# Kernel tuning notes

Hardware: AMD Instinct MI355X
Metric: run time of the kernel (lower is better)

## Reference

```python
import jax, jax.numpy as jnp
import numpy as np


def gcn_conv(x, src, dst, deg_inv_sqrt, W, b):
    # PyG GCNConv: h = x @ W, then symmetric-normalized scatter-add over edges
    # (edge list already includes self-loops; deg computed over it).
    h = x @ W                                   # [N, F_out]
    norm = deg_inv_sqrt[src] * deg_inv_sqrt[dst]  # [E]
    msgs = h[src] * norm[:, None]               # gather + scale
    out = jax.ops.segment_sum(msgs, dst, num_segments=x.shape[0])
    return out + b


def setup_inputs() -> dict:
    key = jax.random.key(0)
    k1, k2, k3, k4 = jax.random.split(key, 4)
    N, E, F_in, F_hid, F_out = 200000, 6400000, 128, 8, 16
    x = jax.random.normal(k1, (N, F_in), dtype=jnp.float32)
    edge_index = jax.random.randint(k2, (2, E), 0, N, dtype=jnp.int64)
    W1 = jax.random.normal(k3, (F_in, F_hid), dtype=jnp.float32) * (1.0 / np.sqrt(F_in))
    b1 = jnp.zeros((F_hid,), dtype=jnp.float32)
    W2 = jax.random.normal(k4, (F_hid, F_out), dtype=jnp.float32) * (1.0 / np.sqrt(F_hid))
    b2 = jnp.zeros((F_out,), dtype=jnp.float32)
    return {"x": x, "edge_index": edge_index, "W1": W1, "b1": b1, "W2": W2, "b2": b2}


def reference(x, edge_index, W1, b1, W2, b2):
    N = x.shape[0]
    # add self-loops (GCNConv default add_self_loops=True)
    loops = jnp.arange(N, dtype=edge_index.dtype)
    src = jnp.concatenate([edge_index[0], loops])
    dst = jnp.concatenate([edge_index[1], loops])
    deg = jax.ops.segment_sum(jnp.ones_like(dst, dtype=x.dtype), dst, num_segments=N)
    deg_inv_sqrt = jnp.where(deg > 0, jax.lax.rsqrt(deg), 0.0)
    h = jax.nn.relu(gcn_conv(x, src, dst, deg_inv_sqrt, W1, b1))
    # dropout is identity in eval mode (training=False)
    out = gcn_conv(h, src, dst, deg_inv_sqrt, W2, b2)
    return out
```

## Files before the change

kernel.cpp:

```cpp
#include <hip/hip_runtime.h>
#include <hip/hip_fp16.h>

#define F_IN  128
#define F_HID 8
#define F_OUT 16

#define SBSH  9
#define SBW   (1 << SBSH)
#define MAXB  400
#define BIN_CAP  32
#define FLUSH_G  16


__global__ void init_gcur(int* __restrict__ gcur, int cap, int B) {
    int b = blockIdx.x * blockDim.x + threadIdx.x;
    if (b < B) gcur[b] = b * cap;
}

__global__ __launch_bounds__(512) void stage_bin(const int* __restrict__ ei,
                                                 int* __restrict__ gcur,
                                                 int* __restrict__ stage,
                                                 int E, int B, int per_block) {
    __shared__ int bin_cnt[MAXB];
    __shared__ int bin_buf[MAXB * BIN_CAP];
    for (int i = threadIdx.x; i < B; i += blockDim.x) bin_cnt[i] = 0;
    __syncthreads();
    const bool vec = ((E & 3) == 0);
    int base = blockIdx.x * per_block;
    int end  = min(E, base + per_block);
    for (int it = base; it < end; it += (int)blockDim.x * 4) {
        int e = it + (int)threadIdx.x * 4;
        int sv[4], dv[4], m4 = 0;
        if (vec && e + 3 < end) {
            int4 s4 = *(const int4*)(ei + e);
            int4 d4 = *(const int4*)(ei + E + e);
            sv[0] = s4.x; sv[1] = s4.y; sv[2] = s4.z; sv[3] = s4.w;
            dv[0] = d4.x; dv[1] = d4.y; dv[2] = d4.z; dv[3] = d4.w;
            m4 = 4;
        } else {
            for (int q = 0; e + q < end && q < 4; q++) { sv[q] = ei[e + q]; dv[q] = ei[E + e + q]; m4++; }
        }
        for (int q = 0; q < m4; q++) {
            int b   = dv[q] >> SBSH;
            int val = (sv[q] << SBSH) | (dv[q] & (SBW - 1));
            int pos = atomicAdd(&bin_cnt[b], 1);
            if (pos < BIN_CAP) {
                bin_buf[b * BIN_CAP + ((pos + b) & (BIN_CAP - 1))] = val;
            } else {
                int gp = atomicAdd(&gcur[b], 1);
                stage[gp] = val;
            }
        }
        __syncthreads();
        for (int b2 = threadIdx.x; b2 < B; b2 += blockDim.x) {
            int c = min(bin_cnt[b2], BIN_CAP);
            if (c >= FLUSH_G) {
                int m = c & ~(FLUSH_G - 1);
                int r = atomicAdd(&gcur[b2], m);
                for (int k = 0; k < m; k++)
                    stage[r + k] = bin_buf[b2 * BIN_CAP + ((k + b2) & (BIN_CAP - 1))];
                for (int k = m; k < c; k++)
                    bin_buf[b2 * BIN_CAP + ((k - m + b2) & (BIN_CAP - 1))] =
                        bin_buf[b2 * BIN_CAP + ((k + b2) & (BIN_CAP - 1))];
                bin_cnt[b2] = c - m;
            } else {
                bin_cnt[b2] = c;
            }
        }
        __syncthreads();
    }
    for (int b2 = threadIdx.x; b2 < B; b2 += blockDim.x) {
        int c = min(bin_cnt[b2], BIN_CAP);
        if (c > 0) {
            int r = atomicAdd(&gcur[b2], c);
            for (int k = 0; k < c; k++)
                stage[r + k] = bin_buf[b2 * BIN_CAP + ((k + b2) & (BIN_CAP - 1))];
        }
    }
}

__global__ __launch_bounds__(512) void scatter_csr(const int* __restrict__ stage,
                                                   const int* __restrict__ gcur,
                                                   int cap,
                                                   int* __restrict__ cnt,
                                                   float* __restrict__ dis,
                                                   int* __restrict__ row_start,
                                                   int* __restrict__ csr, int n) {
    __shared__ int s0[SBW], s1[SBW];
    int b  = blockIdx.x;
    int nb = b << SBSH;
    int i  = threadIdx.x;
    s0[i] = 0;
    __syncthreads();
    int base = b * cap;
    int num  = gcur[b] - base;
    for (int k = i; k < num; k += 512)
        atomicAdd(&s0[stage[base + k] & (SBW - 1)], 1);
    __syncthreads();
    int c = s0[i];
    if (nb + i < n) { cnt[nb + i] = c; dis[nb + i] = rsqrtf((float)(c + 1)); }
    int* src = s0; int* dst = s1;
    for (int off = 1; off < SBW; off <<= 1) {
        int v = src[i] + ((i >= off) ? src[i - off] : 0);
        dst[i] = v;
        __syncthreads();
        int* t = src; src = dst; dst = t;
    }
    int e = base + src[i] - c;
    if (nb + i < n) row_start[nb + i] = e;
    dst[i] = e;
    __syncthreads();
    for (int k = i; k < num; k += 512) {
        int v = stage[base + k];
        int pos = atomicAdd(&dst[v & (SBW - 1)], 1);
        csr[pos] = v >> SBSH;
    }
}

__global__ __launch_bounds__(256) void gemm1(const float* __restrict__ x,
                                             const float* __restrict__ W1,
                                             const float* __restrict__ dis,
                                             __half* __restrict__ g1, int n) {
    __shared__ float w[F_IN * F_HID];
    for (int i = threadIdx.x; i < F_IN * F_HID; i += blockDim.x) w[i] = W1[i];
    __syncthreads();
    int node = blockIdx.x * blockDim.x + threadIdx.x;
    if (node >= n) return;
    const float4* xr = (const float4*)(x + (size_t)node * F_IN);
    float acc[F_HID];
#pragma unroll
    for (int f = 0; f < F_HID; f++) acc[f] = 0.0f;
#pragma unroll
    for (int j = 0; j < F_IN / 4; j++) {
        float4 v = xr[j];
        const float* wr = &w[j * 4 * F_HID];
#pragma unroll
        for (int f = 0; f < F_HID; f++)
            acc[f] += v.x * wr[f] + v.y * wr[F_HID + f] + v.z * wr[2 * F_HID + f] + v.w * wr[3 * F_HID + f];
    }
    float d = dis[node];
    __half2 h[4];
#pragma unroll
    for (int p = 0; p < 4; p++) h[p] = __floats2half2_rn(acc[2 * p] * d, acc[2 * p + 1] * d);
    *(uint4*)(g1 + (size_t)node * F_HID) = *(uint4*)h;
}

__global__ __launch_bounds__(256) void aggregate_relu(const int* __restrict__ csr,
                                                      const int* __restrict__ row_start,
                                                      const int* __restrict__ cnt,
                                                      const float* __restrict__ dis,
                                                      const float* __restrict__ b1,
                                                      const __half* __restrict__ gin,
                                                      __half* __restrict__ gout, int n) {
    __shared__ float bb[F_HID];
    if (threadIdx.x < F_HID) bb[threadIdx.x] = b1[threadIdx.x];
    __syncthreads();
    int t = blockIdx.x * blockDim.x + threadIdx.x;
    int node = t >> 3;
    int f = t & 7;
    if (node >= n) return;
    int beg = row_start[node];
    int c   = cnt[node];
    float acc = __half2float(gin[(size_t)node * F_HID + f]);
    int j = 0;
    for (; j + 3 < c; j += 4) {
        int s0 = __builtin_nontemporal_load(csr + beg + j);
        int s1 = __builtin_nontemporal_load(csr + beg + j + 1);
        int s2 = __builtin_nontemporal_load(csr + beg + j + 2);
        int s3 = __builtin_nontemporal_load(csr + beg + j + 3);
        float a0 = __half2float(gin[(size_t)s0 * F_HID + f]);
        float a1 = __half2float(gin[(size_t)s1 * F_HID + f]);
        float a2 = __half2float(gin[(size_t)s2 * F_HID + f]);
        float a3 = __half2float(gin[(size_t)s3 * F_HID + f]);
        acc += (a0 + a1) + (a2 + a3);
    }
    for (; j < c; j++) {
        int s = __builtin_nontemporal_load(csr + beg + j);
        acc += __half2float(gin[(size_t)s * F_HID + f]);
    }
    float d = dis[node];
    float r = fmaxf(acc * d + bb[f], 0.0f) * d;
    gout[(size_t)node * F_HID + f] = __float2half(r);
}

__global__ __launch_bounds__(256) void aggregate_out(const int* __restrict__ csr,
                                                     const int* __restrict__ row_start,
                                                     const int* __restrict__ cnt,
                                                     const float* __restrict__ dis,
                                                     const float* __restrict__ W2,
                                                     const float* __restrict__ b2,
                                                     const __half* __restrict__ gin,
                                                     float* __restrict__ out, int n) {
    __shared__ float w[F_HID * F_OUT];
    __shared__ float bb[F_OUT];
    if (threadIdx.x < F_HID * F_OUT) w[threadIdx.x] = W2[threadIdx.x];
    if (threadIdx.x < F_OUT) bb[threadIdx.x] = b2[threadIdx.x];
    __syncthreads();
    int t = blockIdx.x * blockDim.x + threadIdx.x;
    int node = t >> 3;
    int f = t & 7;
    if (node >= n) return;
    int beg = row_start[node];
    int c   = cnt[node];
    float acc = __half2float(gin[(size_t)node * F_HID + f]);
    int j = 0;
    for (; j + 3 < c; j += 4) {
        int s0 = __builtin_nontemporal_load(csr + beg + j);
        int s1 = __builtin_nontemporal_load(csr + beg + j + 1);
        int s2 = __builtin_nontemporal_load(csr + beg + j + 2);
        int s3 = __builtin_nontemporal_load(csr + beg + j + 3);
        float a0 = __half2float(gin[(size_t)s0 * F_HID + f]);
        float a1 = __half2float(gin[(size_t)s1 * F_HID + f]);
        float a2 = __half2float(gin[(size_t)s2 * F_HID + f]);
        float a3 = __half2float(gin[(size_t)s3 * F_HID + f]);
        acc += (a0 + a1) + (a2 + a3);
    }
    for (; j < c; j++) {
        int s = __builtin_nontemporal_load(csr + beg + j);
        acc += __half2float(gin[(size_t)s * F_HID + f]);
    }
    float a_self = acc * dis[node];
    float o0 = bb[2 * f], o1 = bb[2 * f + 1];
#pragma unroll
    for (int k = 0; k < 8; k++) {
        float ak = __shfl(a_self, k, 8);
        o0 += ak * w[k * F_OUT + 2 * f];
        o1 += ak * w[k * F_OUT + 2 * f + 1];
    }
    *(float2*)(out + (size_t)node * F_OUT + 2 * f) = make_float2(o0, o1);
}

extern "C" void kernel_launch(void* const* d_in, const int* in_sizes, int n_in,
                              void* d_out, int out_size, void* d_ws, size_t ws_size,
                              hipStream_t stream) {
    const float* x  = (const float*)d_in[0];
    const int*   ei = (const int*)d_in[1];
    const float* W1 = (const float*)d_in[2];
    const float* b1 = (const float*)d_in[3];
    const float* W2 = (const float*)d_in[4];
    const float* b2 = (const float*)d_in[5];
    float* out = (float*)d_out;

    const int N = in_sizes[0] / F_IN;
    const int E = in_sizes[1] / 2;
    const int B = (N + SBW - 1) >> SBSH;

    int avg = (E + B - 1) / B;
    int cap = (avg + avg / 16 + 255) & ~255;

    int*    stage     = (int*)d_ws;
    int*    csr       = stage + (size_t)B * cap;
    float*  dis       = (float*)(csr + (size_t)B * cap);
    __half* gA        = (__half*)(dis + N);
    __half* gB        = (__half*)((int*)gA + (size_t)N * 4);
    int*    cnt       = (int*)gB + (size_t)N * 4;
    int*    row_start = cnt + N;
    int*    gcur      = row_start + N;

    const int BT = 256;
    dim3 blkN((N + BT - 1) / BT), thr(BT);
    dim3 blkA(((size_t)N * F_HID + BT - 1) / BT);

    int per_block = ((E + 639) / 640 + 2047) & ~2047;
    int SBLK = (E + per_block - 1) / per_block;

    init_gcur     <<<dim3((B + BT - 1) / BT), thr, 0, stream>>>(gcur, cap, B);
    stage_bin     <<<dim3(SBLK), dim3(512), 0, stream>>>(ei, gcur, stage, E, B, per_block);
    scatter_csr   <<<dim3(B),   dim3(512), 0, stream>>>(stage, gcur, cap, cnt, dis, row_start, csr, N);
    gemm1         <<<blkN, thr, 0, stream>>>(x, W1, dis, gA, N);
    aggregate_relu<<<blkA, thr, 0, stream>>>(csr, row_start, cnt, dis, b1, gA, gB, N);
    aggregate_out <<<blkA, thr, 0, stream>>>(csr, row_start, cnt, dis, W2, b2, gB, out, N);
}
```

Measured before the change: 462.7 us.

## Aggregate directly from binned edge buckets with LDS atomics instead of building CSR

Removes the CSR construction pass (prefix scan plus scatter into csr). Aggregation now streams each destination bucket's packed edges into LDS with double-buffered global_load_lds and accumulates into per-node LDS accumulators using workgroup-scope float atomics. The first GEMM now uses eight threads per node with shuffle reductions, and the degree pass reads int4 vectors. The trade is contended LDS atomics and one block per 512-node bucket, giving limited parallelism (about 391 blocks), in exchange for dropping a full edge-array write and read.

```diff
diff --git a/kernel.cpp b/kernel.cpp
--- a/kernel.cpp
+++ b/kernel.cpp
@@ -10,7 +10,10 @@
 #define MAXB  400
 #define BIN_CAP  32
 #define FLUSH_G  16
-
+#define TILE_E   2048
+
+
+typedef float f32x4 __attribute__((ext_vector_type(4)));
 
 __global__ void init_gcur(int* __restrict__ gcur, int cap, int B) {
     int b = blockIdx.x * blockDim.x + threadIdx.x;
@@ -79,155 +82,194 @@
     }
 }
 
-__global__ __launch_bounds__(512) void scatter_csr(const int* __restrict__ stage,
-                                                   const int* __restrict__ gcur,
-                                                   int cap,
-                                                   int* __restrict__ cnt,
-                                                   float* __restrict__ dis,
-                                                   int* __restrict__ row_start,
-                                                   int* __restrict__ csr, int n) {
-    __shared__ int s0[SBW], s1[SBW];
-    int b  = blockIdx.x;
-    int nb = b << SBSH;
-    int i  = threadIdx.x;
+__global__ __launch_bounds__(512) void degree_dis(const int* __restrict__ stage,
+                                                  const int* __restrict__ gcur,
+                                                  int cap, float* __restrict__ dis, int n) {
+    __shared__ int s0[SBW];
+    int b = blockIdx.x, i = threadIdx.x;
     s0[i] = 0;
     __syncthreads();
     int base = b * cap;
-    int num  = gcur[b] - base;
-    for (int k = i; k < num; k += 512)
+    int num  = min(gcur[b] - base, cap);
+    int numv = num & ~(TILE_E - 1);
+    for (int k = i * 4; k < numv; k += TILE_E) {
+        int4 v = *(const int4*)(stage + base + k);
+        atomicAdd(&s0[v.x & (SBW - 1)], 1);
+        atomicAdd(&s0[v.y & (SBW - 1)], 1);
+        atomicAdd(&s0[v.z & (SBW - 1)], 1);
+        atomicAdd(&s0[v.w & (SBW - 1)], 1);
+    }
+    for (int k = numv + i; k < num; k += 512)
         atomicAdd(&s0[stage[base + k] & (SBW - 1)], 1);
     __syncthreads();
-    int c = s0[i];
-    if (nb + i < n) { cnt[nb + i] = c; dis[nb + i] = rsqrtf((float)(c + 1)); }
-    int* src = s0; int* dst = s1;
-    for (int off = 1; off < SBW; off <<= 1) {
-        int v = src[i] + ((i >= off) ? src[i - off] : 0);
-        dst[i] = v;
-        __syncthreads();
-        int* t = src; src = dst; dst = t;
-    }
-    int e = base + src[i] - c;
-    if (nb + i < n) row_start[nb + i] = e;
-    dst[i] = e;
-    __syncthreads();
-    for (int k = i; k < num; k += 512) {
-        int v = stage[base + k];
-        int pos = atomicAdd(&dst[v & (SBW - 1)], 1);
-        csr[pos] = v >> SBSH;
-    }
+    int node = (b << SBSH) + i;
+    if (node < n) dis[node] = rsqrtf((float)(s0[i] + 1));
 }
 
 __global__ __launch_bounds__(256) void gemm1(const float* __restrict__ x,
                                              const float* __restrict__ W1,
                                              const float* __restrict__ dis,
                                              __half* __restrict__ g1, int n) {
-    __shared__ float w[F_IN * F_HID];
-    for (int i = threadIdx.x; i < F_IN * F_HID; i += blockDim.x) w[i] = W1[i];
-    __syncthreads();
-    int node = blockIdx.x * blockDim.x + threadIdx.x;
+    __shared__ float w2[F_HID * F_IN];
+    for (int i = threadIdx.x; i < F_HID * F_IN; i += blockDim.x) {
+        int f = i >> 7, k = i & (F_IN - 1);
+        w2[i] = W1[k * F_HID + f];
+    }
+    __syncthreads();
+    int t = blockIdx.x * blockDim.x + threadIdx.x;
+    int node = t >> 3, l = t & 7;
     if (node >= n) return;
-    const float4* xr = (const float4*)(x + (size_t)node * F_IN);
+    const f32x4* xr = (const f32x4*)(x + (size_t)node * F_IN);
     float acc[F_HID];
 #pragma unroll
     for (int f = 0; f < F_HID; f++) acc[f] = 0.0f;
 #pragma unroll
-    for (int j = 0; j < F_IN / 4; j++) {
-        float4 v = xr[j];
-        const float* wr = &w[j * 4 * F_HID];
-#pragma unroll
-        for (int f = 0; f < F_HID; f++)
-            acc[f] += v.x * wr[f] + v.y * wr[F_HID + f] + v.z * wr[2 * F_HID + f] + v.w * wr[3 * F_HID + f];
-    }
-    float d = dis[node];
-    __half2 h[4];
-#pragma unroll
-    for (int p = 0; p < 4; p++) h[p] = __floats2half2_rn(acc[2 * p] * d, acc[2 * p + 1] * d);
-    *(uint4*)(g1 + (size_t)node * F_HID) = *(uint4*)h;
-}
-
-__global__ __launch_bounds__(256) void aggregate_relu(const int* __restrict__ csr,
-                                                      const int* __restrict__ row_start,
-                                                      const int* __restrict__ cnt,
-                                                      const float* __restrict__ dis,
-                                                      const float* __restrict__ b1,
-                                                      const __half* __restrict__ gin,
-                                                      __half* __restrict__ gout, int n) {
+    for (int it = 0; it < 4; it++) {
+        int j = l + it * 8;
+        f32x4 v = xr[j];
+#pragma unroll
+        for (int f = 0; f < F_HID; f++) {
+            const float* wf = &w2[f * F_IN + j * 4];
+            acc[f] += v[0] * wf[0] + v[1] * wf[1] + v[2] * wf[2] + v[3] * wf[3];
+        }
+    }
+#pragma unroll
+    for (int f = 0; f < F_HID; f++) {
+        acc[f] += __shfl_xor(acc[f], 1);
+        acc[f] += __shfl_xor(acc[f], 2);
+        acc[f] += __shfl_xor(acc[f], 4);
+    }
+    if (l == 0) {
+        float d = dis[node];
+        __half2 h[4];
+#pragma unroll
+        for (int p = 0; p < 4; p++) h[p] = __floats2half2_rn(acc[2 * p] * d, acc[2 * p + 1] * d);
+        *(uint4*)(g1 + (size_t)node * F_HID) = *(uint4*)h;
+    }
+}
+
+__device__ __forceinline__ void gll16(const int* gsrc, int* ldst) {
+    __builtin_amdgcn_global_load_lds(
+        (const __attribute__((address_space(1))) void*)gsrc,
+        (__attribute__((address_space(3))) void*)ldst, 16, 0, 0);
+}
+
+__device__ __forceinline__ void lds_faddx(float* p, float v) {
+    (void)__hip_atomic_fetch_add(p, v, __ATOMIC_RELAXED, __HIP_MEMORY_SCOPE_WORKGROUP);
+}
+
+__device__ __forceinline__ void stage_tile(const int* __restrict__ stage, int base,
+                                           int t, int* lbuf, int tid) {
+    gll16(stage + base + t * TILE_E + tid * 4, lbuf + ((tid >> 6) << 8));
+}
+
+__device__ __forceinline__ void bucket_accumulate(const int* __restrict__ stage,
+                                                  int base, int num,
+                                                  const __half* __restrict__ gin,
+                                                  float* acc, int* ebuf, int tid) {
+    int ntile = (num + TILE_E - 1) / TILE_E;
+    if (ntile > 0) stage_tile(stage, base, 0, ebuf, tid);
+    int g = tid >> 3, f = tid & 7;
+    for (int t = 0; t < ntile; t++) {
+        int cur = t & 1;
+        __syncthreads();
+        if (t + 1 < ntile) stage_tile(stage, base, t + 1, ebuf + ((cur ^ 1) * TILE_E), tid);
+        int cnt_t = min(TILE_E, num - t * TILE_E);
+        const int* eb = ebuf + cur * TILE_E;
+        int k = g;
+        for (; k + 192 < cnt_t; k += 256) {
+            int v0 = eb[k], v1 = eb[k + 64], v2 = eb[k + 128], v3 = eb[k + 192];
+            float a0 = __half2float(gin[(size_t)((unsigned)v0 >> SBSH) * F_HID + f]);
+            float a1 = __half2float(gin[(size_t)((unsigned)v1 >> SBSH) * F_HID + f]);
+            float a2 = __half2float(gin[(size_t)((unsigned)v2 >> SBSH) * F_HID + f]);
+            float a3 = __half2float(gin[(size_t)((unsigned)v3 >> SBSH) * F_HID + f]);
+            lds_faddx(&acc[(v0 & (SBW - 1)) * F_HID + f], a0);
+            lds_faddx(&acc[(v1 & (SBW - 1)) * F_HID + f], a1);
+            lds_faddx(&acc[(v2 & (SBW - 1)) * F_HID + f], a2);
+            lds_faddx(&acc[(v3 & (SBW - 1)) * F_HID + f], a3);
+        }
+        for (; k < cnt_t; k += 64) {
+            int v = eb[k];
+            float a = __half2float(gin[(size_t)((unsigned)v >> SBSH) * F_HID + f]);
+            lds_faddx(&acc[(v & (SBW - 1)) * F_HID + f], a);
+        }
+    }
+    __syncthreads();
+}
+
+__global__ __launch_bounds__(512) void agg1(const int* __restrict__ stage,
+                                            const int* __restrict__ gcur, int cap,
+                                            const float* __restrict__ dis,
+                                            const float* __restrict__ b1,
+                                            const __half* __restrict__ gin,
+                                            __half* __restrict__ gout, int n) {
+    __shared__ __align__(16) float acc[SBW * F_HID];
+    __shared__ __align__(16) int   ebuf[2 * TILE_E];
     __shared__ float bb[F_HID];
-    if (threadIdx.x < F_HID) bb[threadIdx.x] = b1[threadIdx.x];
-    __syncthreads();
-    int t = blockIdx.x * blockDim.x + threadIdx.x;
-    int node = t >> 3;
-    int f = t & 7;
-    if (node >= n) return;
-    int beg = row_start[node];
-    int c   = cnt[node];
-    float acc = __half2float(gin[(size_t)node * F_HID + f]);
-    int j = 0;
-    for (; j + 3 < c; j += 4) {
-        int s0 = __builtin_nontemporal_load(csr + beg + j);
-        int s1 = __builtin_nontemporal_load(csr + beg + j + 1);
-        int s2 = __builtin_nontemporal_load(csr + beg + j + 2);
-        int s3 = __builtin_nontemporal_load(csr + beg + j + 3);
-        float a0 = __half2float(gin[(size_t)s0 * F_HID + f]);
-        float a1 = __half2float(gin[(size_t)s1 * F_HID + f]);
-        float a2 = __half2float(gin[(size_t)s2 * F_HID + f]);
-        float a3 = __half2float(gin[(size_t)s3 * F_HID + f]);
-        acc += (a0 + a1) + (a2 + a3);
-    }
-    for (; j < c; j++) {
-        int s = __builtin_nontemporal_load(csr + beg + j);
-        acc += __half2float(gin[(size_t)s * F_HID + f]);
-    }
-    float d = dis[node];
-    float r = fmaxf(acc * d + bb[f], 0.0f) * d;
-    gout[(size_t)node * F_HID + f] = __float2half(r);
-}
-
-__global__ __launch_bounds__(256) void aggregate_out(const int* __restrict__ csr,
-                                                     const int* __restrict__ row_start,
-                                                     const int* __restrict__ cnt,
-                                                     const float* __restrict__ dis,
-                                                     const float* __restrict__ W2,
-                                                     const float* __restrict__ b2,
-                                                     const __half* __restrict__ gin,
-                                                     float* __restrict__ out, int n) {
+    int tid = threadIdx.x, b = blockIdx.x;
+    if (tid < F_HID) bb[tid] = b1[tid];
+#pragma unroll
+    for (int q = 0; q < (SBW * F_HID) / 512; q++) acc[tid + q * 512] = 0.0f;
+    int base = b * cap;
+    int num  = min(gcur[b] - base, cap);
+    bucket_accumulate(stage, base, num, gin, acc, ebuf, tid);
+    int node = (b << SBSH) + tid;
+    if (node < n) {
+        float d = dis[node];
+        uint4 hv = *(const uint4*)(gin + (size_t)node * F_HID);
+        __half hbuf[F_HID]; *(uint4*)hbuf = hv;
+        __half ob[F_HID];
+#pragma unroll
+        for (int f2 = 0; f2 < F_HID; f2++) {
+            float s = acc[tid * F_HID + f2] + __half2float(hbuf[f2]);
+            ob[f2] = __float2half(fmaxf(fmaf(d, s, bb[f2]), 0.0f) * d);
+        }
+        *(uint4*)(gout + (size_t)node * F_HID) = *(uint4*)ob;
+    }
+}
+
+__global__ __launch_bounds__(512) void agg2(const int* __restrict__ stage,
+                                            const int* __restrict__ gcur, int cap,
+                                            const float* __restrict__ dis,
+                                            const float* __restrict__ W2,
+                                            const float* __restrict__ b2,
+                                            const __half* __restrict__ gin,
+                                            float* __restrict__ out, int n) {
+    __shared__ __align__(16) float acc[SBW * F_HID];
+    __shared__ __align__(16) int   ebuf[2 * TILE_E];
     __shared__ float w[F_HID * F_OUT];
     __shared__ float bb[F_OUT];
-    if (threadIdx.x < F_HID * F_OUT) w[threadIdx.x] = W2[threadIdx.x];
-    if (threadIdx.x < F_OUT) bb[threadIdx.x] = b2[threadIdx.x];
-    __syncthreads();
-    int t = blockIdx.x * blockDim.x + threadIdx.x;
-    int node = t >> 3;
-    int f = t & 7;
-    if (node >= n) return;
-    int beg = row_start[node];
-    int c   = cnt[node];
-    float acc = __half2float(gin[(size_t)node * F_HID + f]);
-    int j = 0;
-    for (; j + 3 < c; j += 4) {
-        int s0 = __builtin_nontemporal_load(csr + beg + j);
-        int s1 = __builtin_nontemporal_load(csr + beg + j + 1);
-        int s2 = __builtin_nontemporal_load(csr + beg + j + 2);
-        int s3 = __builtin_nontemporal_load(csr + beg + j + 3);
-        float a0 = __half2float(gin[(size_t)s0 * F_HID + f]);
-        float a1 = __half2float(gin[(size_t)s1 * F_HID + f]);
-        float a2 = __half2float(gin[(size_t)s2 * F_HID + f]);
-        float a3 = __half2float(gin[(size_t)s3 * F_HID + f]);
-        acc += (a0 + a1) + (a2 + a3);
-    }
-    for (; j < c; j++) {
-        int s = __builtin_nontemporal_load(csr + beg + j);
-        acc += __half2float(gin[(size_t)s * F_HID + f]);
-    }
-    float a_self = acc * dis[node];
-    float o0 = bb[2 * f], o1 = bb[2 * f + 1];
-#pragma unroll
-    for (int k = 0; k < 8; k++) {
-        float ak = __shfl(a_self, k, 8);
-        o0 += ak * w[k * F_OUT + 2 * f];
-        o1 += ak * w[k * F_OUT + 2 * f + 1];
-    }
-    *(float2*)(out + (size_t)node * F_OUT + 2 * f) = make_float2(o0, o1);
+    int tid = threadIdx.x, b = blockIdx.x;
+    if (tid < F_HID * F_OUT) w[tid] = W2[tid];
+    if (tid < F_OUT) bb[tid] = b2[tid];
+#pragma unroll
+    for (int q = 0; q < (SBW * F_HID) / 512; q++) acc[tid + q * 512] = 0.0f;
+    int base = b * cap;
+    int num  = min(gcur[b] - base, cap);
+    bucket_accumulate(stage, base, num, gin, acc, ebuf, tid);
+    int node = (b << SBSH) + tid;
+    if (node < n) {
+        float d = dis[node];
+        uint4 hv = *(const uint4*)(gin + (size_t)node * F_HID);
+        __half hbuf[F_HID]; *(uint4*)hbuf = hv;
+        float a[F_HID];
+#pragma unroll
+        for (int f2 = 0; f2 < F_HID; f2++)
+            a[f2] = d * (acc[tid * F_HID + f2] + __half2float(hbuf[f2]));
+        float o[F_OUT];
+#pragma unroll
+        for (int oo = 0; oo < F_OUT; oo++) o[oo] = bb[oo];
+#pragma unroll
+        for (int f2 = 0; f2 < F_HID; f2++)
+#pragma unroll
+            for (int oo = 0; oo < F_OUT; oo++)
+                o[oo] = fmaf(a[f2], w[f2 * F_OUT + oo], o[oo]);
+        float4* op = (float4*)(out + (size_t)node * F_OUT);
+        op[0] = make_float4(o[0],  o[1],  o[2],  o[3]);
+        op[1] = make_float4(o[4],  o[5],  o[6],  o[7]);
+        op[2] = make_float4(o[8],  o[9],  o[10], o[11]);
+        op[3] = make_float4(o[12], o[13], o[14], o[15]);
+    }
 }
 
 extern "C" void kernel_launch(void* const* d_in, const int* in_sizes, int n_in,
@@ -248,26 +290,21 @@
     int avg = (E + B - 1) / B;
     int cap = (avg + avg / 16 + 255) & ~255;
 
-    int*    stage     = (int*)d_ws;
-    int*    csr       = stage + (size_t)B * cap;
-    float*  dis       = (float*)(csr + (size_t)B * cap);
-    __half* gA        = (__half*)(dis + N);
-    __half* gB        = (__half*)((int*)gA + (size_t)N * 4);
-    int*    cnt       = (int*)gB + (size_t)N * 4;
-    int*    row_start = cnt + N;
-    int*    gcur      = row_start + N;
+    int*    stage = (int*)d_ws;
+    float*  dis   = (float*)(stage + (size_t)B * cap + TILE_E);
+    __half* gA    = (__half*)(dis + N);
+    __half* gB    = gA + (size_t)N * F_HID;
+    int*    gcur  = (int*)(gB + (size_t)N * F_HID);
 
     const int BT = 256;
-    dim3 blkN((N + BT - 1) / BT), thr(BT);
-    dim3 blkA(((size_t)N * F_HID + BT - 1) / BT);
 
     int per_block = ((E + 639) / 640 + 2047) & ~2047;
     int SBLK = (E + per_block - 1) / per_block;
 
-    init_gcur     <<<dim3((B + BT - 1) / BT), thr, 0, stream>>>(gcur, cap, B);
-    stage_bin     <<<dim3(SBLK), dim3(512), 0, stream>>>(ei, gcur, stage, E, B, per_block);
-    scatter_csr   <<<dim3(B),   dim3(512), 0, stream>>>(stage, gcur, cap, cnt, dis, row_start, csr, N);
-    gemm1         <<<blkN, thr, 0, stream>>>(x, W1, dis, gA, N);
-    aggregate_relu<<<blkA, thr, 0, stream>>>(csr, row_start, cnt, dis, b1, gA, gB, N);
-    aggregate_out <<<blkA, thr, 0, stream>>>(csr, row_start, cnt, dis, W2, b2, gB, out, N);
-}
+    init_gcur <<<dim3((B + BT - 1) / BT), dim3(BT), 0, stream>>>(gcur, cap, B);
+    stage_bin <<<dim3(SBLK), dim3(512), 0, stream>>>(ei, gcur, stage, E, B, per_block);
+    degree_dis<<<dim3(B), dim3(512), 0, stream>>>(stage, gcur, cap, dis, N);
+    gemm1     <<<dim3(((size_t)N * 8 + BT - 1) / BT), dim3(BT), 0, stream>>>(x, W1, dis, gA, N);
+    agg1      <<<dim3(B), dim3(512), 0, stream>>>(stage, gcur, cap, dis, b1, gA, gB, N);
+    agg2      <<<dim3(B), dim3(512), 0, stream>>>(stage, gcur, cap, dis, W2, b2, gB, out, N);
+}
```

Result: slower. 944.5 us (+104.1%).
